# Performance work log

Measured on AMD Instinct MI355X. Metric: run time of the kernel, lower is better.

Reference implementation:

```python
import jax, jax.numpy as jnp
import numpy as np

T = 22        # TypeEncoder.tensor_size() (assumed)
H = 2         # attention heads
C = 64        # hc_graph (per-head out channels)
L = 3         # num_hops
LEAFCAT = 5   # len(LeafType.valid_categories()) (assumed)
NSIZES = 8    # len(LeafType.valid_sizes()) (assumed)
HL = 64       # hc_linear
HT = 64       # hc_task == hc_leafsize
SLOPE = 0.2   # PyG GATConv negative_slope


def _gat(x, src, dst, W, asrc, adst, b):
    # PyG GATConv (concat=True, dropout=0, self-loops already appended to src/dst)
    N = x.shape[0]
    h = (x @ W).reshape(N, H, C)                      # [N,H,C]
    a_s = jnp.einsum('nhc,hc->nh', h, asrc)            # per-node src score
    a_d = jnp.einsum('nhc,hc->nh', h, adst)            # per-node dst score
    e = jax.nn.leaky_relu(a_s[src] + a_d[dst], SLOPE)  # [E+N,H]
    m = jax.ops.segment_max(e, dst, num_segments=N)
    p = jnp.exp(e - m[dst])
    s = jax.ops.segment_sum(p, dst, num_segments=N)
    alpha = p / (s[dst] + 1e-16)                       # scatter-softmax over in-edges
    out = jax.ops.segment_sum(h[src] * alpha[:, :, None], dst, num_segments=N)
    return out.reshape(N, H * C) + b


def _mlp2(z, W1, b1, W2, b2):
    return jax.nn.relu(z @ W1 + b1) @ W2 + b2


def setup_inputs() -> dict:
    key = jax.random.key(0)
    ks = jax.random.split(key, 32)
    N, E, NG, NPG = 102400, 1228800, 256, 400
    D = H * C
    g = lambda k, shp, fan: (jax.random.normal(k, shp, jnp.float32) / np.sqrt(fan)).astype(jnp.float32)
    z = lambda *shp: jnp.zeros(shp, jnp.float32)
    return {
        'x': jax.random.normal(ks[0], (N, D), jnp.float32),
        'edge_index': jax.random.randint(ks[1], (2, E), 0, N),
        'batch': jnp.repeat(jnp.arange(NG, dtype=jnp.int32), NPG),
        'gat_W': g(ks[2], (L, D, D), D),
        'gat_asrc': g(ks[3], (L, H, C), C),
        'gat_adst': g(ks[4], (L, H, C), C),
        'gat_b': z(L, D),
        'shared_W': g(ks[5], (D + T, HL), D + T),
        'shared_b': z(HL),
        'ptr_W1': g(ks[6], (3, HL, HT), HL), 'ptr_b1': z(3, HT),
        'ptr_W2': g(ks[7], (3, HT, 3), HT), 'ptr_b2': z(3, 3),
        'cat_W1': g(ks[8], (HL, HT), HL), 'cat_b1': z(HT),
        'cat_W2': g(ks[9], (HT, LEAFCAT), HT), 'cat_b2': z(LEAFCAT),
        'sf_W1': g(ks[10], (2, HL, HT), HL), 'sf_b1': z(2, HT),
        'sf_W2': g(ks[11], (2, HT, 1), HT), 'sf_b2': z(2, 1),
        'bool_W1': g(ks[12], (HL + T + LEAFCAT + 2, HT), HL + T + LEAFCAT + 2), 'bool_b1': z(HT),
        'bool_W2': g(ks[13], (HT, 1), HT), 'bool_b2': z(1),
        'size_W1': g(ks[14], (HL + T + LEAFCAT + 3, HT), HL + T + LEAFCAT + 3), 'size_b1': z(HT),
        'size_W2': g(ks[15], (HT, NSIZES), HT), 'size_b2': z(NSIZES),
    }


def reference(x, edge_index, batch, gat_W, gat_asrc, gat_adst, gat_b,
              shared_W, shared_b, ptr_W1, ptr_b1, ptr_W2, ptr_b2,
              cat_W1, cat_b1, cat_W2, cat_b2, sf_W1, sf_b1, sf_W2, sf_b2,
              bool_W1, bool_b1, bool_W2, bool_b2, size_W1, size_b1, size_W2, size_b2):
    N = x.shape[0]
    num_graphs = int(batch[-1]) + 1                    # batch is sorted per-graph ids
    node0 = jnp.searchsorted(batch, jnp.arange(num_graphs))  # first node of each graph
    dtype_vec = x[node0, :T]                           # NodeEncoder.split_node_vec dtype slice
    loops = jnp.arange(N)
    src = jnp.concatenate([edge_index[0], loops])      # GATConv add_self_loops=True
    dst = jnp.concatenate([edge_index[1], loops])
    h = x
    for l in range(L):
        h = _gat(h, src, dst, gat_W[l], gat_asrc[l], gat_adst[l], gat_b[l])
        if l < L - 1:
            h = jax.nn.relu(h)
    zf = jax.nn.relu(jnp.concatenate([h[node0], dtype_vec], axis=1) @ shared_W + shared_b)
    # 3 pointer heads, batched
    p = jax.nn.relu(jnp.einsum('gh,khd->kgd', zf, ptr_W1) + ptr_b1[:, None, :])
    ptr = jnp.einsum('kgd,kdo->kgo', p, ptr_W2) + ptr_b2[:, None, :]
    cat_logits = _mlp2(zf, cat_W1, cat_b1, cat_W2, cat_b2)
    q = jax.nn.relu(jnp.einsum('gh,khd->kgd', zf, sf_W1) + sf_b1[:, None, :])
    sf = jnp.einsum('kgd,kdo->kgo', q, sf_W2) + sf_b2[:, None, :]
    signed, floating = sf[0], sf[1]
    bool_in = jnp.concatenate([zf, dtype_vec, cat_logits, signed, floating], axis=1)
    bool_logit = _mlp2(bool_in, bool_W1, bool_b1, bool_W2, bool_b2)
    size_in = jnp.concatenate([bool_in, bool_logit], axis=1)
    size_logits = _mlp2(size_in, size_W1, size_b1, size_W2, size_b2)
    return (ptr[0], ptr[1], ptr[2], cat_logits, signed, floating, bool_logit, size_logits)
```

## Files before the change

kernel.cpp:

```cpp
#include <hip/hip_runtime.h>
#include <hip/hip_bf16.h>

typedef __hip_bfloat16 bf16;
typedef __attribute__((ext_vector_type(8))) short short8;
typedef __attribute__((ext_vector_type(4))) float floatx4;

__device__ __forceinline__ float b2f(bf16 v) { return __bfloat162float(v); }
__device__ __forceinline__ float us2f(unsigned short u) {
    return __uint_as_float(((unsigned)u) << 16);
}
__device__ __forceinline__ unsigned short f2us(float f) {
    bf16 h = __float2bfloat16(f);
    return *(unsigned short*)&h;
}
__device__ __forceinline__ float lo2f(unsigned hv) { return __uint_as_float(hv << 16); }
__device__ __forceinline__ float hi2f(unsigned hv) { return __uint_as_float(hv & 0xffff0000u); }
__device__ __forceinline__ float leaky(float v) { return v > 0.f ? v : 0.2f * v; }

__device__ __forceinline__ float ldw(const void* p, size_t i, int f32) {
    return f32 ? ((const float*)p)[i] : b2f(((const bf16*)p)[i]);
}

template <int F32>
__device__ __forceinline__ float LDWt(const void* p, size_t i) {
    return F32 ? ((const float*)p)[i] : b2f(((const bf16*)p)[i]);
}

__device__ __forceinline__ int or16(const int* f) {
    int r = 0;
#pragma unroll
    for (int j = 0; j < 16; j++) r |= f[j];
    return r;
}

__device__ __forceinline__ float wsum64(float v) {
#pragma unroll
    for (int m = 1; m <= 32; m <<= 1) v += __shfl_xor(v, m);
    return v;
}

__global__ void k_detect_zero(const void* x, int* flagv, char* zbase, size_t zbytes) {
    int b = blockIdx.x;
    int t = threadIdx.x;
    if (b < 16) {
        __shared__ int sbad;
        if (t == 0) sbad = 0;
        __syncthreads();
        float v = b2f(((const bf16*)x)[b * 256 + t]);
        if (!(fabsf(v) < 1e10f)) sbad = 1;
        __syncthreads();
        if (t == 0) flagv[b] = sbad;
    } else {
        size_t off = (size_t)(b - 16) * 4096 + (size_t)t * 16;
        if (off < zbytes) *(uint4*)(zbase + off) = make_uint4(0u, 0u, 0u, 0u);
    }
}

__global__ void k_prep_fused(const void* __restrict__ x, unsigned short* __restrict__ Ab,
                             int nvec,
                             const void* __restrict__ gw, unsigned short* __restrict__ Wt,
                             const void* as_, const void* ad_, const void* b_,
                             float* asF, float* adF, float* bF,
                             const int* __restrict__ batch, int* __restrict__ node0,
                             unsigned char* __restrict__ rootb,
                             unsigned char* __restrict__ flag2, int N,
                             const int* __restrict__ flagv, int nbx8) {
    int b = blockIdx.x;
    int t = threadIdx.x;
    int f32 = or16(flagv);
    if (b < nbx8) {
        int i = b * 256 + t;
        if (i < nvec) {
            if (!f32) {
                ((uint4*)Ab)[i] = ((const uint4*)x)[i];
            } else {
                float4 a = ((const float4*)x)[2 * i];
                float4 c = ((const float4*)x)[2 * i + 1];
                uint4 o;
                o.x = ((unsigned)f2us(a.y) << 16) | f2us(a.x);
                o.y = ((unsigned)f2us(a.w) << 16) | f2us(a.z);
                o.z = ((unsigned)f2us(c.y) << 16) | f2us(c.x);
                o.w = ((unsigned)f2us(c.w) << 16) | f2us(c.z);
                ((uint4*)Ab)[i] = o;
            }
        }
    } else if (b < nbx8 + 192) {
        int i = (b - nbx8) * 256 + t;
        int l = i >> 14, rem = i & 16383, n = rem >> 7, k = rem & 127;
        Wt[i] = f2us(ldw(gw, (size_t)l * 16384 + (size_t)k * 128 + n, f32));
    } else if (b < nbx8 + 194) {
        int i = (b - nbx8 - 192) * 256 + t;
        if (i < 384) {
            asF[i] = ldw(as_, i, f32);
            adF[i] = ldw(ad_, i, f32);
            bF[i] = ldw(b_, i, f32);
        }
    } else {
        int i = (b - nbx8 - 194) * 256 + t;
        if (i < N) {
            int bb = batch[i];
            if (i == 0 || batch[i - 1] != bb) {
                node0[bb] = i;
                rootb[i] = 1;
                flag2[i] = 1;
            }
        }
    }
}

__global__ void k_scan3x(const int* __restrict__ counts,
                         const unsigned char* __restrict__ flag1,
                         const unsigned char* __restrict__ flag2,
                         int* __restrict__ offs, int* __restrict__ wp1, int* __restrict__ wp2,
                         int* __restrict__ bsums, int n) {
    __shared__ int s[256];
    int tid = threadIdx.x;
    int i = blockIdx.x * 256 + tid;
#pragma unroll
    for (int a = 0; a < 3; a++) {
        int v = 0;
        if (i < n) v = (a == 0) ? counts[i] : (a == 1) ? (int)flag1[i] : (int)flag2[i];
        s[tid] = v;
        __syncthreads();
        for (int d = 1; d < 256; d <<= 1) {
            int t2 = (tid >= d) ? s[tid - d] : 0;
            __syncthreads();
            s[tid] += t2;
            __syncthreads();
        }
        int incl = s[tid];
        if (i < n) {
// ... 10 lines not shown
    __shared__ int s[512];
    int tid = threadIdx.x;
#pragma unroll
    for (int a = 0; a < 3; a++) {
        int* arr = bsums + a * 512;
        int v = (tid < nb) ? arr[tid] : 0;
        s[tid] = v;
        __syncthreads();
        for (int d = 1; d < 512; d <<= 1) {
            int t2 = (tid >= d) ? s[tid - d] : 0;
            __syncthreads();
            s[tid] += t2;
            __syncthreads();
        }
        arr[tid] = s[tid] - v;
        if (a >= 1 && tid == 511) nact[a - 1] = s[511];
        __syncthreads();
    }
}

__global__ void k_mark1(const int* __restrict__ ei, const unsigned char* __restrict__ flag2,
                        unsigned char* __restrict__ flag1, int E, int N, int eBlocks) {
    int b = blockIdx.x;
    if (b < eBlocks) {
        int e = b * 256 + threadIdx.x;
        if (e < E && flag2[ei[E + e]]) flag1[ei[e]] = 1;
    } else {
        int i = (b - eBlocks) * 256 + threadIdx.x;
        if (i < N && flag2[i]) flag1[i] = 1;
    }
}

__global__ void k_hist_masked(const int* __restrict__ ei, const unsigned char* __restrict__ flag1,
                              int* __restrict__ counts, int* __restrict__ rank, int E) {
    int e = blockIdx.x * blockDim.x + threadIdx.x;
    if (e < E) {
        int d = ei[E + e];
        if (flag1[d]) rank[e] = atomicAdd(&counts[d], 1);
    }
}

__global__ void k_scatter_wl(const int* __restrict__ ei, const int* __restrict__ offs,
                             const int* __restrict__ bsums, const int* __restrict__ rank,
                             const unsigned char* __restrict__ flag1,
                             const unsigned char* __restrict__ flag2,
                             const int* __restrict__ wp1, const int* __restrict__ wp2,
                             int* __restrict__ adj, int* __restrict__ wl1, int* __restrict__ wl2,
                             int E, int N, int sBlocks) {
    int b = blockIdx.x;
    if (b < sBlocks) {
        int xcd = b & 7;
        int e = (b >> 3) * 256 + threadIdx.x;
        if (e >= E) return;
        int d = ei[E + e];
        if (!flag1[d]) return;
        int lo = (int)(((long long)N * xcd) >> 3);
        int hi = (int)(((long long)N * (xcd + 1)) >> 3);
        if (d >= lo && d < hi) adj[offs[d] + bsums[d >> 8] + rank[e]] = ei[e];
    } else {
        int i = (b - sBlocks) * 256 + threadIdx.x;
        if (i < N) {
            if (flag1[i]) wl1[wp1[i] + bsums[512 + (i >> 8)]] = i;
            if (flag2[i]) wl2[wp2[i] + bsums[1024 + (i >> 8)]] = i;
        }
    }
}

__device__ __forceinline__ void gemm_body(
    const unsigned short* __restrict__ Ab, const unsigned short* __restrict__ Wt,
    unsigned short* __restrict__ Bb, float4* __restrict__ asadv,
    const float* __restrict__ asF, const float* __restrict__ adF, int N,
    const int* __restrict__ wl, const int* __restrict__ nactp, int bb) {
    __shared__ __align__(16) unsigned short Ws[128 * 136];
    __shared__ __align__(16) unsigned short Cs[64 * 136];

    int t = threadIdx.x;
    int r0 = bb * 64;
    int nact = wl ? *nactp : N;
    if (r0 >= nact) return;

    {
        const uint4* src = (const uint4*)Wt;
#pragma unroll
        for (int k = 0; k < 8; k++) {
            int j = t + k * 256;
            int row = j >> 4, c16 = j & 15;
            *(uint4*)&Ws[row * 136 + c16 * 8] = src[j];
        }
    }
    __syncthreads();

    int lane = t & 63;
    int w = t >> 6;
    int ln = lane & 15;
    int quad = lane >> 4;

    int idx = r0 + w * 16 + ln;
    bool valid = idx < nact;
    int arow = idx < N ? idx : N - 1;
    if (wl) arow = valid ? wl[idx] : 0;
    bool wave_active = __any((int)valid);

    if (wave_active) {
        const unsigned short* ap = Ab + (size_t)arow * 128 + quad * 8;

        short8 afrag[4];
        if (valid) {
#pragma unroll
            for (int kt = 0; kt < 4; kt++)
                afrag[kt] = *(const short8*)(ap + kt * 32);
        } else {
#pragma unroll
            for (int kt = 0; kt < 4; kt++)
                afrag[kt] = (short8){0, 0, 0, 0, 0, 0, 0, 0};
        }

        floatx4 acc[8];
#pragma unroll
        for (int nt = 0; nt < 8; nt++) acc[nt] = (floatx4){0.f, 0.f, 0.f, 0.f};

#pragma unroll
        for (int nt = 0; nt < 8; nt++) {
            const unsigned short* wp = Ws + (nt * 16 + ln) * 136 + quad * 8;
#pragma unroll
            for (int kt = 0; kt < 4; kt++) {
                short8 bfrag = *(const short8*)(wp + kt * 32);
                acc[nt] = __builtin_amdgcn_mfma_f32_16x16x32_bf16(afrag[kt], bfrag, acc[nt], 0, 0, 0);
            }
        }

        float as0[4] = {0, 0, 0, 0}, as1[4] = {0, 0, 0, 0};
        float ad0[4] = {0, 0, 0, 0}, ad1[4] = {0, 0, 0, 0};
#pragma unroll
        for (int nt = 0; nt < 8; nt++) {
            float asc = asF[nt * 16 + ln];
            float adc = adF[nt * 16 + ln];
#pragma unroll
            for (int r = 0; r < 4; r++) {
                float v = acc[nt][r];
                Cs[(w * 16 + quad * 4 + r) * 136 + nt * 16 + ln] = f2us(v);
                if (nt < 4) { as0[r] += v * asc; ad0[r] += v * adc; }
                else        { as1[r] += v * asc; ad1[r] += v * adc; }
            }
        }
#pragma unroll
        for (int mask = 1; mask <= 8; mask <<= 1) {
#pragma unroll
            for (int r = 0; r < 4; r++) {
                as0[r] += __shfl_xor(as0[r], mask);
                as1[r] += __shfl_xor(as1[r], mask);
                ad0[r] += __shfl_xor(ad0[r], mask);
                ad1[r] += __shfl_xor(ad1[r], mask);
            }
        }
        if (ln == 0) {
#pragma unroll
            for (int r = 0; r < 4; r++) {
                int idx3 = r0 + w * 16 + quad * 4 + r;
                if (idx3 < nact) {
                    int row = wl ? wl[idx3] : idx3;
// ... 18 lines not shown
}

__global__ __launch_bounds__(256) void k_gemm_mfma(
    const unsigned short* __restrict__ Ab, const unsigned short* __restrict__ Wt,
    unsigned short* __restrict__ Bb, float4* __restrict__ asadv,
    const float* __restrict__ asF, const float* __restrict__ adF, int N,
    const int* __restrict__ wl, const int* __restrict__ nactp) {
    gemm_body(Ab, Wt, Bb, asadv, asF, adF, N, wl, nactp, blockIdx.x);
}

__global__ __launch_bounds__(256) void k_gemm0_mark(
    const unsigned short* __restrict__ Ab, const unsigned short* __restrict__ Wt,
    unsigned short* __restrict__ Bb, float4* __restrict__ asadv,
    const float* __restrict__ asF, const float* __restrict__ adF, int N,
    const int* __restrict__ ei, const unsigned char* __restrict__ rootb,
    unsigned char* __restrict__ flag2, int E, int markBlocks) {
    int b = blockIdx.x;
    if (b < markBlocks) {
        int e = b * 256 + threadIdx.x;
        if (e < E) {
            int d = ei[E + e];
            if (rootb[d]) flag2[ei[e]] = 1;
        }
        return;
    }
    gemm_body(Ab, Wt, Bb, asadv, asF, adF, N, nullptr, nullptr, b - markBlocks);
}

__global__ void k_gat_agg(const uint2* __restrict__ Bu2, const float4* __restrict__ asadv,
                          const int* __restrict__ offs, const int* __restrict__ bsums,
                          const int* __restrict__ counts,
                          const int* __restrict__ adj, const float* __restrict__ biasF,
                          uint2* __restrict__ Au2, float2* __restrict__ pE,
                          const int* __restrict__ nactp, int dorelu,
                          const int* __restrict__ wl) {
    int wave = (blockIdx.x * blockDim.x + threadIdx.x) >> 6;
    int lane = threadIdx.x & 63;
    int hl = lane & 31;
    int hb = lane & 32;
    int idx = wave * 2 + (lane >> 5);
    if (idx >= *nactp) return;
    int node = wl[idx];
    int head = hl >> 4;

    float4 self = asadv[node];
    float ad0 = self.z, ad1 = self.w;
    float es0 = __expf(leaky(self.x + ad0));
    float es1 = __expf(leaky(self.y + ad1));

    int o = offs[node] + bsums[node >> 8];
    int c = counts[node];
    uint2 hvs = Bu2[(size_t)node * 32 + hl];
    float acc0, acc1, acc2, acc3;

    if (c <= 32) {
        int src_r = 0;
        float p0 = 0.f, p1 = 0.f;
        if (hl < c) {
            src_r = adj[o + hl];
            float4 av = asadv[src_r];
            p0 = __expf(leaky(av.x + ad0));
            p1 = __expf(leaky(av.y + ad1));
        }
        float t0 = p0, t1 = p1;
#pragma unroll
        for (int mask = 1; mask <= 16; mask <<= 1) {
            t0 += __shfl_xor(t0, mask);
            t1 += __shfl_xor(t1, mask);
        }
        float inv0 = 1.f / (es0 + t0 + 1e-16f);
        float inv1 = 1.f / (es1 + t1 + 1e-16f);
        p0 *= inv0;
        p1 *= inv1;
        float aself = head ? es1 * inv1 : es0 * inv0;
        acc0 = aself * lo2f(hvs.x);
        acc1 = aself * hi2f(hvs.x);
        acc2 = aself * lo2f(hvs.y);
        acc3 = aself * hi2f(hvs.y);

        uint2 hq[4];
#pragma unroll
        for (int j = 0; j < 4; j++) {
            int s2 = __shfl(src_r, hb + j);
            hq[j] = make_uint2(0u, 0u);
            if (j < c) hq[j] = Bu2[(size_t)s2 * 32 + hl];
        }

        for (int base = 0; base < c; base += 4) {
            uint2 cur[4];
            float av4[4];
#pragma unroll
            for (int j = 0; j < 4; j++) {
                cur[j] = hq[j];
                int idx2 = (base + j) & 31;
                float a0 = __shfl(p0, hb + idx2);
                float a1 = __shfl(p1, hb + idx2);
                float a = head ? a1 : a0;
                av4[j] = (base + j < c) ? a : 0.f;
            }
#pragma unroll
            for (int j = 0; j < 4; j++) {
                int nx = base + 4 + j;
                int s2 = __shfl(src_r, hb + (nx & 31));
                if (nx < c) hq[j] = Bu2[(size_t)s2 * 32 + hl];
            }
#pragma unroll
            for (int j = 0; j < 4; j++) {
                acc0 += av4[j] * lo2f(cur[j].x);
                acc1 += av4[j] * hi2f(cur[j].x);
                acc2 += av4[j] * lo2f(cur[j].y);
                acc3 += av4[j] * hi2f(cur[j].y);
            }
        }
    } else {
        float sum0 = es0, sum1 = es1;
        for (int base = 0; base < c; base += 32) {
            int i = base + hl;
            float p0 = 0.f, p1 = 0.f;
            if (i < c) {
                int s = adj[o + i];
                float4 av = asadv[s];
                p0 = __expf(leaky(av.x + ad0));
                p1 = __expf(leaky(av.y + ad1));
                pE[o + i] = make_float2(p0, p1);
            }
            float t0 = p0, t1 = p1;
#pragma unroll
            for (int mask = 1; mask <= 16; mask <<= 1) {
                t0 += __shfl_xor(t0, mask);
                t1 += __shfl_xor(t1, mask);
            }
            sum0 += t0; sum1 += t1;
        }
        float inv0 = 1.f / (sum0 + 1e-16f);
        float inv1 = 1.f / (sum1 + 1e-16f);
        float aself = head ? es1 * inv1 : es0 * inv0;
        float invh = head ? inv1 : inv0;
        acc0 = aself * lo2f(hvs.x);
        acc1 = aself * hi2f(hvs.x);
        acc2 = aself * lo2f(hvs.y);
        acc3 = aself * hi2f(hvs.y);
        for (int i = 0; i < c; i++) {
            int s = adj[o + i];
            float2 pp = pE[o + i];
            uint2 hv = Bu2[(size_t)s * 32 + hl];
            float a = (head ? pp.y : pp.x) * invh;
            acc0 += a * lo2f(hv.x);
            acc1 += a * hi2f(hv.x);
            acc2 += a * lo2f(hv.y);
            acc3 += a * hi2f(hv.y);
        }
    }

    float4 bb4 = ((const float4*)biasF)[hl];
    float q0 = acc0 + bb4.x;
    float q1 = acc1 + bb4.y;
    float q2 = acc2 + bb4.z;
    float q3 = acc3 + bb4.w;
    if (dorelu) {
        q0 = fmaxf(q0, 0.f); q1 = fmaxf(q1, 0.f);
        q2 = fmaxf(q2, 0.f); q3 = fmaxf(q3, 0.f);
    }
    Au2[(size_t)node * 32 + hl] =
        make_uint2(((unsigned)f2us(q1) << 16) | f2us(q0),
                   ((unsigned)f2us(q3) << 16) | f2us(q2));
}

template <int F32>
__device__ void heads_body(
    const unsigned* __restrict__ Brow, const float4* __restrict__ asadv,
    const int* __restrict__ offs, const int* __restrict__ bsums,
    const int* __restrict__ counts, const int* __restrict__ adj,
    const float* __restrict__ biasF, const int* __restrict__ node0,
    const void* __restrict__ x,
    const void* sW, const void* sb,
    const void* pW1, const void* pb1, const void* pW2, const void* pb2,
    const void* cW1, const void* cb1, const void* cW2, const void* cb2,
    const void* fW1, const void* fb1, const void* fW2, const void* fb2,
    const void* bW1, const void* bb1, const void* bW2, const void* bb2,
    const void* zW1, const void* zb1, const void* zW2, const void* zb2,
    void* __restrict__ outv) {
    int lane = threadIdx.x & 63;
    int g = blockIdx.x * 4 + (threadIdx.x >> 6);
    bf16* outb = (bf16*)outv;
    float* outf = (float*)outv;
#define STORE(idx, val) do { if (F32) outf[idx] = (val); else outb[idx] = __float2bfloat16(val); } while (0)

    int n0 = node0[g];

    float4 self = asadv[n0];
    float es0 = __expf(leaky(self.x + self.z));
    float es1 = __expf(leaky(self.y + self.w));
    int o = offs[n0] + bsums[n0 >> 8];
    int c = counts[n0];

    int srcl = 0;
    float p0 = 0.f, p1 = 0.f;
    if (lane < c) {
        srcl = adj[o + lane];
        float4 av = asadv[srcl];
        p0 = __expf(leaky(av.x + self.z));
        p1 = __expf(leaky(av.y + self.w));
    }
    float sum0 = es0 + wsum64(p0);
    float sum1 = es1 + wsum64(p1);
    for (int base = 64; base < c; base += 64) {
        float q0 = 0.f, q1 = 0.f;
        if (base + lane < c) {
            int s = adj[o + base + lane];
            float4 av = asadv[s];
            q0 = __expf(leaky(av.x + self.z));
            q1 = __expf(leaky(av.y + self.w));
        }
        sum0 += wsum64(q0);
        sum1 += wsum64(q1);
    }
    float inv0 = 1.f / (sum0 + 1e-16f);
    float inv1 = 1.f / (sum1 + 1e-16f);
    float invh = (lane < 32) ? inv0 : inv1;

    unsigned hv0 = Brow[(size_t)n0 * 64 + lane];
    float aself = ((lane < 32) ? es0 : es1) * invh;
    float h0 = aself * lo2f(hv0);
    float h1 = aself * hi2f(hv0);
    int cc = min(c, 64);
    for (int j = 0; j < cc; ++j) {
        int s = __shfl(srcl, j);
        float a0 = __shfl(p0, j);
        float a1 = __shfl(p1, j);
        float aa = ((lane < 32) ? a0 : a1) * invh;
        unsigned hv = Brow[(size_t)s * 64 + lane];
        h0 += aa * lo2f(hv);
        h1 += aa * hi2f(hv);
    }
    for (int j = 64; j < c; ++j) {
        int s = adj[o + j];
        float4 av = asadv[s];
        float aa = (lane < 32) ? __expf(leaky(av.x + self.z)) * inv0
                               : __expf(leaky(av.y + self.w)) * inv1;
        unsigned hv = Brow[(size_t)s * 64 + lane];
        h0 += aa * lo2f(hv);
        h1 += aa * hi2f(hv);
    }
    float2 bias2 = ((const float2*)biasF)[lane];
    h0 += bias2.x;
    h1 += bias2.y;

    float rD = (lane < 22) ? LDWt<F32>(x, (size_t)n0 * 128 + lane) : 0.f;

    float p = 0.f;
    for (int i = 0; i < 64; ++i) {
        p += __shfl(h0, i) * LDWt<F32>(sW, (size_t)(2 * i) * 64 + lane);
        p += __shfl(h1, i) * LDWt<F32>(sW, (size_t)(2 * i + 1) * 64 + lane);
    }
    for (int i = 0; i < 22; ++i)
        p += __shfl(rD, i) * LDWt<F32>(sW, (size_t)(128 + i) * 64 + lane);
    float zf = fmaxf(p + LDWt<F32>(sb, lane), 0.f);

    float bin1 = (lane < 22) ? rD : 0.f;

#pragma unroll
    for (int k = 0; k < 3; ++k) {
        float pp = 0.f;
        for (int i = 0; i < 64; ++i)
            pp += __shfl(zf, i) * LDWt<F32>(pW1, (size_t)k * 4096 + (size_t)i * 64 + lane);
        float tt = fmaxf(pp + LDWt<F32>(pb1, k * 64 + lane), 0.f);
#pragma unroll
        for (int o2 = 0; o2 < 3; ++o2) {
            float v = wsum64(tt * LDWt<F32>(pW2, (size_t)k * 192 + (size_t)lane * 3 + o2));
            if (lane == 0) STORE(k * 768 + g * 3 + o2, v + LDWt<F32>(pb2, k * 3 + o2));
        }
    }

    {
        float pp = 0.f;
        for (int i = 0; i < 64; ++i)
            pp += __shfl(zf, i) * LDWt<F32>(cW1, (size_t)i * 64 + lane);
        float tt = fmaxf(pp + LDWt<F32>(cb1, lane), 0.f);
#pragma unroll
        for (int o2 = 0; o2 < 5; ++o2) {
            float v = wsum64(tt * LDWt<F32>(cW2, (size_t)lane * 5 + o2)) + LDWt<F32>(cb2, o2);
            bin1 = (lane == 22 + o2) ? v : bin1;
            if (lane == 0) STORE(2304 + g * 5 + o2, v);
        }
    }

#pragma unroll
    for (int k = 0; k < 2; ++k) {
        float pp = 0.f;
        for (int i = 0; i < 64; ++i)
            pp += __shfl(zf, i) * LDWt<F32>(fW1, (size_t)k * 4096 + (size_t)i * 64 + lane);
        float tt = fmaxf(pp + LDWt<F32>(fb1, k * 64 + lane), 0.f);
        float v = wsum64(tt * LDWt<F32>(fW2, k * 64 + lane)) + LDWt<F32>(fb2, k);
        bin1 = (lane == 27 + k) ? v : bin1;
        if (lane == 0) STORE(3584 + k * 256 + g, v);
    }

    {
        float pp = 0.f;
        for (int i = 0; i < 64; ++i)
            pp += __shfl(zf, i) * LDWt<F32>(bW1, (size_t)i * 64 + lane);
        for (int i = 0; i < 29; ++i)
            pp += __shfl(bin1, i) * LDWt<F32>(bW1, (size_t)(64 + i) * 64 + lane);
        float tt = fmaxf(pp + LDWt<F32>(bb1, lane), 0.f);
        float v = wsum64(tt * LDWt<F32>(bW2, lane)) + LDWt<F32>(bb2, 0);
        bin1 = (lane == 29) ? v : bin1;
        if (lane == 0) STORE(4096 + g, v);
    }

    {
        float pp = 0.f;
        for (int i = 0; i < 64; ++i)
            pp += __shfl(zf, i) * LDWt<F32>(zW1, (size_t)i * 64 + lane);
        for (int i = 0; i < 30; ++i)
            pp += __shfl(bin1, i) * LDWt<F32>(zW1, (size_t)(64 + i) * 64 + lane);
        float tt = fmaxf(pp + LDWt<F32>(zb1, lane), 0.f);
#pragma unroll
        for (int o2 = 0; o2 < 8; ++o2) {
            float v = wsum64(tt * LDWt<F32>(zW2, (size_t)lane * 8 + o2));
            if (lane == 0) STORE(4352 + g * 8 + o2, v + LDWt<F32>(zb2, o2));
        }
    }
#undef STORE
}

__global__ __launch_bounds__(256) void k_heads2(
    const unsigned* __restrict__ Brow, const float4* __restrict__ asadv,
    const int* __restrict__ offs, const int* __restrict__ bsums,
    const int* __restrict__ counts, const int* __restrict__ adj,
    const float* __restrict__ biasF, const int* __restrict__ node0,
    const void* __restrict__ x,
    const void* sW, const void* sb,
    const void* pW1, const void* pb1, const void* pW2, const void* pb2,
    const void* cW1, const void* cb1, const void* cW2, const void* cb2,
    const void* fW1, const void* fb1, const void* fW2, const void* fb2,
    const void* bW1, const void* bb1, const void* bW2, const void* bb2,
    const void* zW1, const void* zb1, const void* zW2, const void* zb2,
    void* __restrict__ outv, const int* __restrict__ flagv) {
    if (or16(flagv))
        heads_body<1>(Brow, asadv, offs, bsums, counts, adj, biasF, node0, x,
                      sW, sb, pW1, pb1, pW2, pb2, cW1, cb1, cW2, cb2,
                      fW1, fb1, fW2, fb2, bW1, bb1, bW2, bb2,
                      zW1, zb1, zW2, zb2, outv);
    else
        heads_body<0>(Brow, asadv, offs, bsums, counts, adj, biasF, node0, x,
                      sW, sb, pW1, pb1, pW2, pb2, cW1, cb1, cW2, cb2,
                      fW1, fb1, fW2, fb2, bW1, bb1, bW2, bb2,
                      zW1, zb1, zW2, zb2, outv);
}


extern "C" void kernel_launch(void* const* d_in, const int* in_sizes, int n_in,
                              void* d_out, int out_size, void* d_ws, size_t ws_size,
                              hipStream_t stream) {
    const void* x     = d_in[0];
    const int*  ei    = (const int*)d_in[1];
    const int*  batch = (const int*)d_in[2];

    int N = in_sizes[0] / 128;
    int E = in_sizes[1] / 2;

    char* w = (char*)d_ws;
    float4* asad = (float4*)w;              w += (size_t)N * 16;
    unsigned short* A = (unsigned short*)w; w += (size_t)N * 128 * 2;
    unsigned short* B = (unsigned short*)w; w += (size_t)N * 128 * 2;
    float2* pE = (float2*)w;                w += (size_t)E * 8;
    unsigned short* Wt = (unsigned short*)w; w += 3 * 16384 * 2;
    float* asF = (float*)w;                 w += 384 * 4;
    float* adF = (float*)w;                 w += 384 * 4;
    float* bF = (float*)w;                  w += 384 * 4;
    int* offs = (int*)w;                    w += (size_t)N * 4;
    int* wp1 = (int*)w;                     w += (size_t)N * 4;
    int* wp2 = (int*)w;                     w += (size_t)N * 4;
    int* wl1 = (int*)w;                     w += (size_t)N * 4;
    int* wl2 = (int*)w;                     w += (size_t)N * 4;
    int* rank = (int*)w;                    w += (size_t)E * 4;
    int* adj = (int*)w;                     w += (size_t)E * 4;
    int* bsums = (int*)w;                   w += 3 * 512 * 4;
    int* node0 = (int*)w;                   w += 256 * 4;
    int* nact = (int*)w;                    w += 64;
    char* zbase = w;
    int* counts = (int*)w;                  w += (size_t)N * 4;
    unsigned char* flag1 = (unsigned char*)w; w += (size_t)N;
    unsigned char* flag2 = (unsigned char*)w; w += (size_t)N;
    unsigned char* rootb = (unsigned char*)w; w += (size_t)N;
    size_t zbytes = (size_t)N * 7;
    int* flagv = (int*)w;                   w += 64;

    int nb = (N + 255) / 256;
    int nvec = N * 16;
    int nbx8 = (nvec + 255) / 256;
    int nbE = (E + 255) / 256;
    int gemmBlocks = (N + 63) / 64;
    int zBlocks = (int)((zbytes + 4095) / 4096);

    k_detect_zero<<<16 + zBlocks, 256, 0, stream>>>(x, flagv, zbase, zbytes);

    k_prep_fused<<<nbx8 + 194 + nb, 256, 0, stream>>>(
        x, A, nvec, d_in[3], Wt, d_in[4], d_in[5], d_in[6],
        asF, adF, bF, batch, node0, rootb, flag2, N, flagv, nbx8);

    k_gemm0_mark<<<nbE + gemmBlocks, 256, 0, stream>>>(
        A, Wt, B, asad, asF, adF, N, ei, rootb, flag2, E, nbE);

    k_mark1<<<nbE + nb, 256, 0, stream>>>(ei, flag2, flag1, E, N, nbE);

    k_hist_masked<<<nbE, 256, 0, stream>>>(ei, flag1, counts, rank, E);

    k_scan3x<<<nb, 256, 0, stream>>>(counts, flag1, flag2, offs, wp1, wp2, bsums, N);
    k_scan2x<<<1, 512, 0, stream>>>(bsums, nb, nact);

    int sBlocks = 8 * nbE;
    k_scatter_wl<<<sBlocks + nb, 256, 0, stream>>>(
        ei, offs, bsums, rank, flag1, flag2, wp1, wp2, adj, wl1, wl2, E, N, sBlocks);

    int nwaves = (N + 1) / 2;
    int aggblocks = (nwaves + 3) / 4;

    k_gat_agg<<<aggblocks, 256, 0, stream>>>(
        (const uint2*)B, asad, offs, bsums, counts, adj, bF, (uint2*)A, pE,
        nact, 1, wl1);

    k_gemm_mfma<<<gemmBlocks, 256, 0, stream>>>(
        A, Wt + 16384, B, asad, asF + 128, adF + 128, N, wl1, nact);
    k_gat_agg<<<aggblocks, 256, 0, stream>>>(
        (const uint2*)B, asad, offs, bsums, counts, adj, bF + 128, (uint2*)A, pE,
        nact + 1, 1, wl2);

    k_gemm_mfma<<<gemmBlocks, 256, 0, stream>>>(
        A, Wt + 2 * 16384, B, asad, asF + 256, adF + 256, N, wl2, nact + 1);

    k_heads2<<<64, 256, 0, stream>>>(
        (const unsigned*)B, asad, offs, bsums, counts, adj, bF + 256, node0, x,
        d_in[7], d_in[8], d_in[9], d_in[10], d_in[11], d_in[12],
        d_in[13], d_in[14], d_in[15], d_in[16],
        d_in[17], d_in[18], d_in[19], d_in[20],
        d_in[21], d_in[22], d_in[23], d_in[24],
        d_in[25], d_in[26], d_in[27], d_in[28],
        d_out, flagv);
}
```

Baseline: 346.4 us.

## Run output heads as MFMA GEMMs and scatter adjacency with atomic cursors

The per-graph scalar head MLPs become batched bf16 MFMA GEMMs over 64 graphs per block. Head weights are pre-transposed and padded into a bf16 buffer during prep, and the last-layer root aggregation is reused from the generic GAT aggregation kernel writing into a compact buffer. The CSR scatter drops the precomputed rank array and the 8x XCD-partitioned launch in favour of a per-destination atomic cursor. This trades deterministic adjacency order and fp32 head precision for less memory traffic and higher head throughput.

```diff
diff --git a/kernel.cpp b/kernel.cpp
--- a/kernel.cpp
+++ b/kernel.cpp
@@ -5,10 +5,9 @@
 typedef __attribute__((ext_vector_type(8))) short short8;
 typedef __attribute__((ext_vector_type(4))) float floatx4;
 
+#define MF(a, b, c) __builtin_amdgcn_mfma_f32_16x16x32_bf16(a, b, c, 0, 0, 0)
+
 __device__ __forceinline__ float b2f(bf16 v) { return __bfloat162float(v); }
-__device__ __forceinline__ float us2f(unsigned short u) {
-    return __uint_as_float(((unsigned)u) << 16);
-}
 __device__ __forceinline__ unsigned short f2us(float f) {
     bf16 h = __float2bfloat16(f);
     return *(unsigned short*)&h;
@@ -33,10 +32,11 @@
     return r;
 }
 
-__device__ __forceinline__ float wsum64(float v) {
-#pragma unroll
-    for (int m = 1; m <= 32; m <<= 1) v += __shfl_xor(v, m);
-    return v;
+__device__ __forceinline__ void quadred(float part[4]) {
+#pragma unroll
+    for (int m = 1; m <= 8; m <<= 1)
+#pragma unroll
+        for (int r = 0; r < 4; r++) part[r] += __shfl_xor(part[r], m);
 }
 
 __global__ void k_detect_zero(const void* x, int* flagv, char* zbase, size_t zbytes) {
@@ -61,6 +61,9 @@
                              const void* __restrict__ gw, unsigned short* __restrict__ Wt,
                              const void* as_, const void* ad_, const void* b_,
                              float* asF, float* adF, float* bF,
+                             const void* sW_, const void* pW1_, const void* cW1_,
+                             const void* fW1_, const void* bW1_, const void* zW1_,
+                             unsigned short* __restrict__ Whd,
                              const int* __restrict__ batch, int* __restrict__ node0,
                              unsigned char* __restrict__ rootb,
                              unsigned char* __restrict__ flag2, int N,
@@ -95,8 +98,36 @@
             adF[i] = ldw(ad_, i, f32);
             bF[i] = ldw(b_, i, f32);
         }
+    } else if (b < nbx8 + 194 + 184) {
+        int i = (b - nbx8 - 194) * 256 + t;
+        float v;
+        if (i < 10240) {
+            int n = i / 160, k = i - n * 160;
+            v = (k < 150) ? ldw(sW_, (size_t)k * 64 + n, f32) : 0.f;
+        } else if (i < 22528) {
+            int j = i - 10240;
+            int kk = j >> 12, r = j & 4095, n = r >> 6, k = r & 63;
+            v = ldw(pW1_, (size_t)kk * 4096 + (size_t)k * 64 + n, f32);
+        } else if (i < 26624) {
+            int j = i - 22528;
+            int n = j >> 6, k = j & 63;
+            v = ldw(cW1_, (size_t)k * 64 + n, f32);
+        } else if (i < 34816) {
+            int j = i - 26624;
+            int kk = j >> 12, r = j & 4095, n = r >> 6, k = r & 63;
+            v = ldw(fW1_, (size_t)kk * 4096 + (size_t)k * 64 + n, f32);
+        } else if (i < 40960) {
+            int j = i - 34816;
+            int n = j / 96, k = j - n * 96;
+            v = (k < 93) ? ldw(bW1_, (size_t)k * 64 + n, f32) : 0.f;
+        } else {
+            int j = i - 40960;
+            int n = j / 96, k = j - n * 96;
+            v = (k < 94) ? ldw(zW1_, (size_t)k * 64 + n, f32) : 0.f;
+        }
+        Whd[i] = f2us(v);
     } else {
-        int i = (b - nbx8 - 194) * 256 + t;
+        int i = (b - nbx8 - 194 - 184) * 256 + t;
         if (i < N) {
             int bb = batch[i];
             if (i == 0 || batch[i - 1] != bb) {
@@ -173,33 +204,31 @@
 }
 
 __global__ void k_hist_masked(const int* __restrict__ ei, const unsigned char* __restrict__ flag1,
-                              int* __restrict__ counts, int* __restrict__ rank, int E) {
+                              int* __restrict__ counts, int E) {
     int e = blockIdx.x * blockDim.x + threadIdx.x;
     if (e < E) {
         int d = ei[E + e];
-        if (flag1[d]) rank[e] = atomicAdd(&counts[d], 1);
+        if (flag1[d]) atomicAdd(&counts[d], 1);
     }
 }
 
 __global__ void k_scatter_wl(const int* __restrict__ ei, const int* __restrict__ offs,
-                             const int* __restrict__ bsums, const int* __restrict__ rank,
+                             const int* __restrict__ bsums, int* __restrict__ cur,
                              const unsigned char* __restrict__ flag1,
                              const unsigned char* __restrict__ flag2,
                              const int* __restrict__ wp1, const int* __restrict__ wp2,
                              int* __restrict__ adj, int* __restrict__ wl1, int* __restrict__ wl2,
-                             int E, int N, int sBlocks) {
+                             int E, int N, int eBlocks) {
     int b = blockIdx.x;
-    if (b < sBlocks) {
-        int xcd = b & 7;
-        int e = (b >> 3) * 256 + threadIdx.x;
+    if (b < eBlocks) {
+        int e = b * 256 + threadIdx.x;
         if (e >= E) return;
         int d = ei[E + e];
         if (!flag1[d]) return;
-        int lo = (int)(((long long)N * xcd) >> 3);
-        int hi = (int)(((long long)N * (xcd + 1)) >> 3);
-        if (d >= lo && d < hi) adj[offs[d] + bsums[d >> 8] + rank[e]] = ei[e];
+        int r = atomicAdd(&cur[d], 1);
+        adj[offs[d] + bsums[d >> 8] + r] = ei[e];
     } else {
-        int i = (b - sBlocks) * 256 + threadIdx.x;
+        int i = (b - eBlocks) * 256 + threadIdx.x;
         if (i < N) {
             if (flag1[i]) wl1[wp1[i] + bsums[512 + (i >> 8)]] = i;
             if (flag2[i]) wl2[wp2[i] + bsums[1024 + (i >> 8)]] = i;
@@ -266,7 +295,7 @@
 #pragma unroll
             for (int kt = 0; kt < 4; kt++) {
                 short8 bfrag = *(const short8*)(wp + kt * 32);
-                acc[nt] = __builtin_amdgcn_mfma_f32_16x16x32_bf16(afrag[kt], bfrag, acc[nt], 0, 0, 0);
+                acc[nt] = MF(afrag[kt], bfrag, acc[nt]);
             }
         }
 
@@ -351,14 +380,15 @@
                           const int* __restrict__ counts,
                           const int* __restrict__ adj, const float* __restrict__ biasF,
                           uint2* __restrict__ Au2, float2* __restrict__ pE,
-                          const int* __restrict__ nactp, int dorelu,
+                          const int* __restrict__ nactp, int nfix, int dorelu, int byidx,
                           const int* __restrict__ wl) {
     int wave = (blockIdx.x * blockDim.x + threadIdx.x) >> 6;
     int lane = threadIdx.x & 63;
     int hl = lane & 31;
     int hb = lane & 32;
     int idx = wave * 2 + (lane >> 5);
-    if (idx >= *nactp) return;
+    int n = nfix ? nfix : *nactp;
+    if (idx >= n) return;
     int node = wl[idx];
     int head = hl >> 4;
 
@@ -406,11 +436,11 @@
         }
 
         for (int base = 0; base < c; base += 4) {
-            uint2 cur[4];
+            uint2 cu[4];
             float av4[4];
 #pragma unroll
             for (int j = 0; j < 4; j++) {
-                cur[j] = hq[j];
+                cu[j] = hq[j];
                 int idx2 = (base + j) & 31;
                 float a0 = __shfl(p0, hb + idx2);
                 float a1 = __shfl(p1, hb + idx2);
@@ -425,10 +455,10 @@
             }
 #pragma unroll
             for (int j = 0; j < 4; j++) {
-                acc0 += av4[j] * lo2f(cur[j].x);
-                acc1 += av4[j] * hi2f(cur[j].x);
-                acc2 += av4[j] * lo2f(cur[j].y);
-                acc3 += av4[j] * hi2f(cur[j].y);
+                acc0 += av4[j] * lo2f(cu[j].x);
+                acc1 += av4[j] * hi2f(cu[j].x);
+                acc2 += av4[j] * lo2f(cu[j].y);
+                acc3 += av4[j] * hi2f(cu[j].y);
             }
         }
     } else {
@@ -480,192 +510,281 @@
         q0 = fmaxf(q0, 0.f); q1 = fmaxf(q1, 0.f);
         q2 = fmaxf(q2, 0.f); q3 = fmaxf(q3, 0.f);
     }
-    Au2[(size_t)node * 32 + hl] =
+    Au2[(size_t)(byidx ? idx : node) * 32 + hl] =
         make_uint2(((unsigned)f2us(q1) << 16) | f2us(q0),
                    ((unsigned)f2us(q3) << 16) | f2us(q2));
 }
 
 template <int F32>
-__device__ void heads_body(
-    const unsigned* __restrict__ Brow, const float4* __restrict__ asadv,
-    const int* __restrict__ offs, const int* __restrict__ bsums,
-    const int* __restrict__ counts, const int* __restrict__ adj,
-    const float* __restrict__ biasF, const int* __restrict__ node0,
-    const void* __restrict__ x,
-    const void* sW, const void* sb,
-    const void* pW1, const void* pb1, const void* pW2, const void* pb2,
-    const void* cW1, const void* cb1, const void* cW2, const void* cb2,
-    const void* fW1, const void* fb1, const void* fW2, const void* fb2,
-    const void* bW1, const void* bb1, const void* bW2, const void* bb2,
-    const void* zW1, const void* zb1, const void* zW2, const void* zb2,
+__device__ void heads_mfma_body(
+    const unsigned* __restrict__ hroot32, const void* __restrict__ x,
+    const int* __restrict__ node0, const unsigned short* __restrict__ Whd,
+    const void* sb, const void* pb1, const void* pW2, const void* pb2,
+    const void* cb1, const void* cW2, const void* cb2,
+    const void* fb1, const void* fW2, const void* fb2,
+    const void* bb1, const void* bW2, const void* bb2,
+    const void* zb1, const void* zW2, const void* zb2,
     void* __restrict__ outv) {
-    int lane = threadIdx.x & 63;
-    int g = blockIdx.x * 4 + (threadIdx.x >> 6);
+    __shared__ __align__(16) unsigned short hinS[64 * 168];
+    __shared__ __align__(16) unsigned short TwS[4][16 * 168];
+
+    int t = threadIdx.x;
+    int g0b = blockIdx.x * 64;
     bf16* outb = (bf16*)outv;
     float* outf = (float*)outv;
 #define STORE(idx, val) do { if (F32) outf[idx] = (val); else outb[idx] = __float2bfloat16(val); } while (0)
 
-    int n0 = node0[g];
-
-    float4 self = asadv[n0];
-    float es0 = __expf(leaky(self.x + self.z));
-    float es1 = __expf(leaky(self.y + self.w));
-    int o = offs[n0] + bsums[n0 >> 8];
-    int c = counts[n0];
-
-    int srcl = 0;
-    float p0 = 0.f, p1 = 0.f;
-    if (lane < c) {
-        srcl = adj[o + lane];
-        float4 av = asadv[srcl];
-        p0 = __expf(leaky(av.x + self.z));
-        p1 = __expf(leaky(av.y + self.w));
-    }
-    float sum0 = es0 + wsum64(p0);
-    float sum1 = es1 + wsum64(p1);
-    for (int base = 64; base < c; base += 64) {
-        float q0 = 0.f, q1 = 0.f;
-        if (base + lane < c) {
-            int s = adj[o + base + lane];
-            float4 av = asadv[s];
-            q0 = __expf(leaky(av.x + self.z));
-            q1 = __expf(leaky(av.y + self.w));
-        }
-        sum0 += wsum64(q0);
-        sum1 += wsum64(q1);
-    }
-    float inv0 = 1.f / (sum0 + 1e-16f);
-    float inv1 = 1.f / (sum1 + 1e-16f);
-    float invh = (lane < 32) ? inv0 : inv1;
-
-    unsigned hv0 = Brow[(size_t)n0 * 64 + lane];
-    float aself = ((lane < 32) ? es0 : es1) * invh;
-    float h0 = aself * lo2f(hv0);
-    float h1 = aself * hi2f(hv0);
-    int cc = min(c, 64);
-    for (int j = 0; j < cc; ++j) {
-        int s = __shfl(srcl, j);
-        float a0 = __shfl(p0, j);
-        float a1 = __shfl(p1, j);
-        float aa = ((lane < 32) ? a0 : a1) * invh;
-        unsigned hv = Brow[(size_t)s * 64 + lane];
-        h0 += aa * lo2f(hv);
-        h1 += aa * hi2f(hv);
-    }
-    for (int j = 64; j < c; ++j) {
-        int s = adj[o + j];
-        float4 av = asadv[s];
-        float aa = (lane < 32) ? __expf(leaky(av.x + self.z)) * inv0
-                               : __expf(leaky(av.y + self.w)) * inv1;
-        unsigned hv = Brow[(size_t)s * 64 + lane];
-        h0 += aa * lo2f(hv);
-        h1 += aa * hi2f(hv);
-    }
-    float2 bias2 = ((const float2*)biasF)[lane];
-    h0 += bias2.x;
-    h1 += bias2.y;
-
-    float rD = (lane < 22) ? LDWt<F32>(x, (size_t)n0 * 128 + lane) : 0.f;
-
-    float p = 0.f;
-    for (int i = 0; i < 64; ++i) {
-        p += __shfl(h0, i) * LDWt<F32>(sW, (size_t)(2 * i) * 64 + lane);
-        p += __shfl(h1, i) * LDWt<F32>(sW, (size_t)(2 * i + 1) * 64 + lane);
-    }
-    for (int i = 0; i < 22; ++i)
-        p += __shfl(rD, i) * LDWt<F32>(sW, (size_t)(128 + i) * 64 + lane);
-    float zf = fmaxf(p + LDWt<F32>(sb, lane), 0.f);
-
-    float bin1 = (lane < 22) ? rD : 0.f;
-
-#pragma unroll
-    for (int k = 0; k < 3; ++k) {
-        float pp = 0.f;
-        for (int i = 0; i < 64; ++i)
-            pp += __shfl(zf, i) * LDWt<F32>(pW1, (size_t)k * 4096 + (size_t)i * 64 + lane);
-        float tt = fmaxf(pp + LDWt<F32>(pb1, k * 64 + lane), 0.f);
-#pragma unroll
-        for (int o2 = 0; o2 < 3; ++o2) {
-            float v = wsum64(tt * LDWt<F32>(pW2, (size_t)k * 192 + (size_t)lane * 3 + o2));
-            if (lane == 0) STORE(k * 768 + g * 3 + o2, v + LDWt<F32>(pb2, k * 3 + o2));
-        }
-    }
-
     {
-        float pp = 0.f;
-        for (int i = 0; i < 64; ++i)
-            pp += __shfl(zf, i) * LDWt<F32>(cW1, (size_t)i * 64 + lane);
-        float tt = fmaxf(pp + LDWt<F32>(cb1, lane), 0.f);
-#pragma unroll
-        for (int o2 = 0; o2 < 5; ++o2) {
-            float v = wsum64(tt * LDWt<F32>(cW2, (size_t)lane * 5 + o2)) + LDWt<F32>(cb2, o2);
-            bin1 = (lane == 22 + o2) ? v : bin1;
-            if (lane == 0) STORE(2304 + g * 5 + o2, v);
-        }
-    }
-
-#pragma unroll
-    for (int k = 0; k < 2; ++k) {
-        float pp = 0.f;
-        for (int i = 0; i < 64; ++i)
-            pp += __shfl(zf, i) * LDWt<F32>(fW1, (size_t)k * 4096 + (size_t)i * 64 + lane);
-        float tt = fmaxf(pp + LDWt<F32>(fb1, k * 64 + lane), 0.f);
-        float v = wsum64(tt * LDWt<F32>(fW2, k * 64 + lane)) + LDWt<F32>(fb2, k);
-        bin1 = (lane == 27 + k) ? v : bin1;
-        if (lane == 0) STORE(3584 + k * 256 + g, v);
+        unsigned* h32 = (unsigned*)hinS;
+        for (int j = t; j < 64 * 64; j += 256) {
+            int gl = j >> 6, c = j & 63;
+            h32[gl * 84 + c] = hroot32[(size_t)(g0b + gl) * 64 + c];
+        }
+        for (int j = t; j < 64 * 20; j += 256) {
+            int gl = j / 20, c = j - gl * 20;
+            int n0 = node0[g0b + gl];
+            int k0 = 2 * c;
+            float d0 = (k0 < 22) ? LDWt<F32>(x, (size_t)n0 * 128 + k0) : 0.f;
+            float d1 = (k0 + 1 < 22) ? LDWt<F32>(x, (size_t)n0 * 128 + k0 + 1) : 0.f;
+            h32[gl * 84 + 64 + c] = ((unsigned)f2us(d1) << 16) | f2us(d0);
+        }
+    }
+    __syncthreads();
+
+    int w = t >> 6;
+    int lane = t & 63;
+    int ln = lane & 15, quad = lane >> 4;
+    unsigned short* T = TwS[w];
+    int gq = quad * 4;
+    int gw0 = g0b + w * 16;
+
+    for (int j = lane; j < 16 * 32; j += 64) {
+        int gl = j >> 5, c = j & 31;
+        T[gl * 168 + 64 + c] =
+            (c < 22) ? hinS[(w * 16 + gl) * 168 + 128 + c] : (unsigned short)0;
+    }
+
+    short8 afA[5];
+#pragma unroll
+    for (int kt = 0; kt < 5; kt++)
+        afA[kt] = *(const short8*)&hinS[(w * 16 + ln) * 168 + quad * 8 + kt * 32];
+#pragma unroll
+    for (int nt = 0; nt < 4; nt++) {
+        floatx4 acc = (floatx4){0.f, 0.f, 0.f, 0.f};
+        const unsigned short* bp = Whd + (nt * 16 + ln) * 160 + quad * 8;
+#pragma unroll
+        for (int kt = 0; kt < 5; kt++)
+            acc = MF(afA[kt], *(const short8*)(bp + kt * 32), acc);
+        float bias = LDWt<F32>(sb, nt * 16 + ln);
+#pragma unroll
+        for (int r = 0; r < 4; r++)
+            T[(gq + r) * 168 + nt * 16 + ln] = f2us(fmaxf(acc[r] + bias, 0.f));
+    }
+    __syncthreads();
+
+    short8 af20 = *(const short8*)&T[ln * 168 + quad * 8];
+    short8 af21 = *(const short8*)&T[ln * 168 + quad * 8 + 32];
+
+#pragma unroll
+    for (int k = 0; k < 3; k++) {
+        const unsigned short* Bw = Whd + 10240 + k * 4096;
+        floatx4 acc[4];
+#pragma unroll
+        for (int nt = 0; nt < 4; nt++) {
+            floatx4 a = (floatx4){0.f, 0.f, 0.f, 0.f};
+            const unsigned short* bp = Bw + (nt * 16 + ln) * 64 + quad * 8;
+            a = MF(af20, *(const short8*)bp, a);
+            a = MF(af21, *(const short8*)(bp + 32), a);
+            float b1 = LDWt<F32>(pb1, k * 64 + nt * 16 + ln);
+#pragma unroll
+            for (int r = 0; r < 4; r++) a[r] = fmaxf(a[r] + b1, 0.f);
+            acc[nt] = a;
+        }
+#pragma unroll
+        for (int o = 0; o < 3; o++) {
+            float w2[4], part[4];
+#pragma unroll
+            for (int nt = 0; nt < 4; nt++)
+                w2[nt] = LDWt<F32>(pW2, (size_t)k * 192 + (size_t)(nt * 16 + ln) * 3 + o);
+#pragma unroll
+            for (int r = 0; r < 4; r++)
+                part[r] = acc[0][r] * w2[0] + acc[1][r] * w2[1] +
+                          acc[2][r] * w2[2] + acc[3][r] * w2[3];
+            quadred(part);
+            if (ln == 0) {
+                float b2 = LDWt<F32>(pb2, k * 3 + o);
+#pragma unroll
+                for (int r = 0; r < 4; r++)
+                    STORE(k * 768 + (gw0 + gq + r) * 3 + o, part[r] + b2);
+            }
+        }
     }
 
     {
-        float pp = 0.f;
-        for (int i = 0; i < 64; ++i)
-            pp += __shfl(zf, i) * LDWt<F32>(bW1, (size_t)i * 64 + lane);
-        for (int i = 0; i < 29; ++i)
-            pp += __shfl(bin1, i) * LDWt<F32>(bW1, (size_t)(64 + i) * 64 + lane);
-        float tt = fmaxf(pp + LDWt<F32>(bb1, lane), 0.f);
-        float v = wsum64(tt * LDWt<F32>(bW2, lane)) + LDWt<F32>(bb2, 0);
-        bin1 = (lane == 29) ? v : bin1;
-        if (lane == 0) STORE(4096 + g, v);
-    }
+        const unsigned short* Bw = Whd + 22528;
+        floatx4 acc[4];
+#pragma unroll
+        for (int nt = 0; nt < 4; nt++) {
+            floatx4 a = (floatx4){0.f, 0.f, 0.f, 0.f};
+            const unsigned short* bp = Bw + (nt * 16 + ln) * 64 + quad * 8;
+            a = MF(af20, *(const short8*)bp, a);
+            a = MF(af21, *(const short8*)(bp + 32), a);
+            float b1 = LDWt<F32>(cb1, nt * 16 + ln);
+#pragma unroll
+            for (int r = 0; r < 4; r++) a[r] = fmaxf(a[r] + b1, 0.f);
+            acc[nt] = a;
+        }
+#pragma unroll
+        for (int o = 0; o < 5; o++) {
+            float w2[4], part[4];
+#pragma unroll
+            for (int nt = 0; nt < 4; nt++)
+                w2[nt] = LDWt<F32>(cW2, (size_t)(nt * 16 + ln) * 5 + o);
+#pragma unroll
+            for (int r = 0; r < 4; r++)
+                part[r] = acc[0][r] * w2[0] + acc[1][r] * w2[1] +
+                          acc[2][r] * w2[2] + acc[3][r] * w2[3];
+            quadred(part);
+            if (ln == 0) {
+                float b2 = LDWt<F32>(cb2, o);
+#pragma unroll
+                for (int r = 0; r < 4; r++) {
+                    float v = part[r] + b2;
+                    T[(gq + r) * 168 + 86 + o] = f2us(v);
+                    STORE(2304 + (gw0 + gq + r) * 5 + o, v);
+                }
+            }
+        }
+    }
+
+#pragma unroll
+    for (int k = 0; k < 2; k++) {
+        const unsigned short* Bw = Whd + 26624 + k * 4096;
+        floatx4 acc[4];
+#pragma unroll
+        for (int nt = 0; nt < 4; nt++) {
+            floatx4 a = (floatx4){0.f, 0.f, 0.f, 0.f};
+            const unsigned short* bp = Bw + (nt * 16 + ln) * 64 + quad * 8;
+            a = MF(af20, *(const short8*)bp, a);
+            a = MF(af21, *(const short8*)(bp + 32), a);
+            float b1 = LDWt<F32>(fb1, k * 64 + nt * 16 + ln);
+#pragma unroll
+            for (int r = 0; r < 4; r++) a[r] = fmaxf(a[r] + b1, 0.f);
+            acc[nt] = a;
+        }
+        float w2[4], part[4];
+#pragma unroll
+        for (int nt = 0; nt < 4; nt++)
+            w2[nt] = LDWt<F32>(fW2, (size_t)k * 64 + nt * 16 + ln);
+#pragma unroll
+        for (int r = 0; r < 4; r++)
+            part[r] = acc[0][r] * w2[0] + acc[1][r] * w2[1] +
+                      acc[2][r] * w2[2] + acc[3][r] * w2[3];
+        quadred(part);
+        if (ln == 0) {
+            float b2 = LDWt<F32>(fb2, k);
+#pragma unroll
+            for (int r = 0; r < 4; r++) {
+                float v = part[r] + b2;
+                T[(gq + r) * 168 + 91 + k] = f2us(v);
+                STORE(3584 + k * 256 + (gw0 + gq + r), v);
+            }
+        }
+    }
+    __syncthreads();
+
+    short8 af3 = *(const short8*)&T[ln * 168 + 64 + quad * 8];
 
     {
-        float pp = 0.f;
-        for (int i = 0; i < 64; ++i)
-            pp += __shfl(zf, i) * LDWt<F32>(zW1, (size_t)i * 64 + lane);
-        for (int i = 0; i < 30; ++i)
-            pp += __shfl(bin1, i) * LDWt<F32>(zW1, (size_t)(64 + i) * 64 + lane);
-        float tt = fmaxf(pp + LDWt<F32>(zb1, lane), 0.f);
-#pragma unroll
-        for (int o2 = 0; o2 < 8; ++o2) {
-            float v = wsum64(tt * LDWt<F32>(zW2, (size_t)lane * 8 + o2));
-            if (lane == 0) STORE(4352 + g * 8 + o2, v + LDWt<F32>(zb2, o2));
+        const unsigned short* Bw = Whd + 34816;
+        floatx4 acc[4];
+#pragma unroll
+        for (int nt = 0; nt < 4; nt++) {
+            floatx4 a = (floatx4){0.f, 0.f, 0.f, 0.f};
+            const unsigned short* bp = Bw + (nt * 16 + ln) * 96 + quad * 8;
+            a = MF(af20, *(const short8*)bp, a);
+            a = MF(af21, *(const short8*)(bp + 32), a);
+            a = MF(af3, *(const short8*)(bp + 64), a);
+            float b1 = LDWt<F32>(bb1, nt * 16 + ln);
+#pragma unroll
+            for (int r = 0; r < 4; r++) a[r] = fmaxf(a[r] + b1, 0.f);
+            acc[nt] = a;
+        }
+        float w2[4], part[4];
+#pragma unroll
+        for (int nt = 0; nt < 4; nt++)
+            w2[nt] = LDWt<F32>(bW2, nt * 16 + ln);
+#pragma unroll
+        for (int r = 0; r < 4; r++)
+            part[r] = acc[0][r] * w2[0] + acc[1][r] * w2[1] +
+                      acc[2][r] * w2[2] + acc[3][r] * w2[3];
+        quadred(part);
+        if (ln == 0) {
+            float b2 = LDWt<F32>(bb2, 0);
+#pragma unroll
+            for (int r = 0; r < 4; r++) {
+                float v = part[r] + b2;
+                T[(gq + r) * 168 + 93] = f2us(v);
+                STORE(4096 + (gw0 + gq + r), v);
+            }
+        }
+    }
+    __syncthreads();
+
+    af3 = *(const short8*)&T[ln * 168 + 64 + quad * 8];
+
+    {
+        const unsigned short* Bw = Whd + 40960;
+        floatx4 acc[4];
+#pragma unroll
+        for (int nt = 0; nt < 4; nt++) {
+            floatx4 a = (floatx4){0.f, 0.f, 0.f, 0.f};
+            const unsigned short* bp = Bw + (nt * 16 + ln) * 96 + quad * 8;
+            a = MF(af20, *(const short8*)bp, a);
+            a = MF(af21, *(const short8*)(bp + 32), a);
+            a = MF(af3, *(const short8*)(bp + 64), a);
+            float b1 = LDWt<F32>(zb1, nt * 16 + ln);
+#pragma unroll
+            for (int r = 0; r < 4; r++) a[r] = fmaxf(a[r] + b1, 0.f);
+            acc[nt] = a;
+        }
+#pragma unroll
+        for (int o = 0; o < 8; o++) {
+            float w2[4], part[4];
+#pragma unroll
+            for (int nt = 0; nt < 4; nt++)
+                w2[nt] = LDWt<F32>(zW2, (size_t)(nt * 16 + ln) * 8 + o);
+#pragma unroll
+            for (int r = 0; r < 4; r++)
+                part[r] = acc[0][r] * w2[0] + acc[1][r] * w2[1] +
+                          acc[2][r] * w2[2] + acc[3][r] * w2[3];
+            quadred(part);
+            if (ln == 0) {
+                float b2 = LDWt<F32>(zb2, o);
+#pragma unroll
+                for (int r = 0; r < 4; r++)
+                    STORE(4352 + (gw0 + gq + r) * 8 + o, part[r] + b2);
+            }
         }
     }
 #undef STORE
 }
 
-__global__ __launch_bounds__(256) void k_heads2(
-    const unsigned* __restrict__ Brow, const float4* __restrict__ asadv,
-    const int* __restrict__ offs, const int* __restrict__ bsums,
-    const int* __restrict__ counts, const int* __restrict__ adj,
-    const float* __restrict__ biasF, const int* __restrict__ node0,
-    const void* __restrict__ x,
-    const void* sW, const void* sb,
-    const void* pW1, const void* pb1, const void* pW2, const void* pb2,
-    const void* cW1, const void* cb1, const void* cW2, const void* cb2,
-    const void* fW1, const void* fb1, const void* fW2, const void* fb2,
-    const void* bW1, const void* bb1, const void* bW2, const void* bb2,
-    const void* zW1, const void* zb1, const void* zW2, const void* zb2,
+__global__ __launch_bounds__(256) void k_heads_mfma(
+    const unsigned* __restrict__ hroot32, const void* __restrict__ x,
+    const int* __restrict__ node0, const unsigned short* __restrict__ Whd,
+    const void* sb, const void* pb1, const void* pW2, const void* pb2,
+    const void* cb1, const void* cW2, const void* cb2,
+    const void* fb1, const void* fW2, const void* fb2,
+    const void* bb1, const void* bW2, const void* bb2,
+    const void* zb1, const void* zW2, const void* zb2,
     void* __restrict__ outv, const int* __restrict__ flagv) {
     if (or16(flagv))
-        heads_body<1>(Brow, asadv, offs, bsums, counts, adj, biasF, node0, x,
-                      sW, sb, pW1, pb1, pW2, pb2, cW1, cb1, cW2, cb2,
-                      fW1, fb1, fW2, fb2, bW1, bb1, bW2, bb2,
-                      zW1, zb1, zW2, zb2, outv);
+        heads_mfma_body<1>(hroot32, x, node0, Whd, sb, pb1, pW2, pb2, cb1, cW2, cb2,
+                           fb1, fW2, fb2, bb1, bW2, bb2, zb1, zW2, zb2, outv);
     else
-        heads_body<0>(Brow, asadv, offs, bsums, counts, adj, biasF, node0, x,
-                      sW, sb, pW1, pb1, pW2, pb2, cW1, cb1, cW2, cb2,
-                      fW1, fb1, fW2, fb2, bW1, bb1, bW2, bb2,
-                      zW1, zb1, zW2, zb2, outv);
+        heads_mfma_body<0>(hroot32, x, node0, Whd, sb, pb1, pW2, pb2, cb1, cW2, cb2,
+                           fb1, fW2, fb2, bb1, bW2, bb2, zb1, zW2, zb2, outv);
 }
 
 
@@ -685,6 +804,7 @@
     unsigned short* B = (unsigned short*)w; w += (size_t)N * 128 * 2;
     float2* pE = (float2*)w;                w += (size_t)E * 8;
     unsigned short* Wt = (unsigned short*)w; w += 3 * 16384 * 2;
+    unsigned short* Whd = (unsigned short*)w; w += 47104 * 2;
     float* asF = (float*)w;                 w += 384 * 4;
     float* adF = (float*)w;                 w += 384 * 4;
     float* bF = (float*)w;                  w += 384 * 4;
@@ -693,17 +813,18 @@
     int* wp2 = (int*)w;                     w += (size_t)N * 4;
     int* wl1 = (int*)w;                     w += (size_t)N * 4;
     int* wl2 = (int*)w;                     w += (size_t)N * 4;
-    int* rank = (int*)w;                    w += (size_t)E * 4;
     int* adj = (int*)w;                     w += (size_t)E * 4;
     int* bsums = (int*)w;                   w += 3 * 512 * 4;
     int* node0 = (int*)w;                   w += 256 * 4;
     int* nact = (int*)w;                    w += 64;
+    unsigned* hroot = (unsigned*)w;         w += 256 * 128 * 2;
     char* zbase = w;
     int* counts = (int*)w;                  w += (size_t)N * 4;
+    int* cur = (int*)w;                     w += (size_t)N * 4;
     unsigned char* flag1 = (unsigned char*)w; w += (size_t)N;
     unsigned char* flag2 = (unsigned char*)w; w += (size_t)N;
     unsigned char* rootb = (unsigned char*)w; w += (size_t)N;
-    size_t zbytes = (size_t)N * 7;
+    size_t zbytes = (size_t)N * 11;
     int* flagv = (int*)w;                   w += 64;
 
     int nb = (N + 255) / 256;
@@ -715,46 +836,51 @@
 
     k_detect_zero<<<16 + zBlocks, 256, 0, stream>>>(x, flagv, zbase, zbytes);
 
-    k_prep_fused<<<nbx8 + 194 + nb, 256, 0, stream>>>(
+    k_prep_fused<<<nbx8 + 194 + 184 + nb, 256, 0, stream>>>(
         x, A, nvec, d_in[3], Wt, d_in[4], d_in[5], d_in[6],
-        asF, adF, bF, batch, node0, rootb, flag2, N, flagv, nbx8);
+        asF, adF, bF,
+        d_in[7], d_in[9], d_in[13], d_in[17], d_in[21], d_in[25], Whd,
+        batch, node0, rootb, flag2, N, flagv, nbx8);
 
     k_gemm0_mark<<<nbE + gemmBlocks, 256, 0, stream>>>(
         A, Wt, B, asad, asF, adF, N, ei, rootb, flag2, E, nbE);
 
     k_mark1<<<nbE + nb, 256, 0, stream>>>(ei, flag2, flag1, E, N, nbE);
 
-    k_hist_masked<<<nbE, 256, 0, stream>>>(ei, flag1, counts, rank, E);
+    k_hist_masked<<<nbE, 256, 0, stream>>>(ei, flag1, counts, E);
 
     k_scan3x<<<nb, 256, 0, stream>>>(counts, flag1, flag2, offs, wp1, wp2, bsums, N);
     k_scan2x<<<1, 512, 0, stream>>>(bsums, nb, nact);
 
-    int sBlocks = 8 * nbE;
-    k_scatter_wl<<<sBlocks + nb, 256, 0, stream>>>(
-        ei, offs, bsums, rank, flag1, flag2, wp1, wp2, adj, wl1, wl2, E, N, sBlocks);
+    k_scatter_wl<<<nbE + nb, 256, 0, stream>>>(
+        ei, offs, bsums, cur, flag1, flag2, wp1, wp2, adj, wl1, wl2, E, N, nbE);
 
     int nwaves = (N + 1) / 2;
     int aggblocks = (nwaves + 3) / 4;
 
     k_gat_agg<<<aggblocks, 256, 0, stream>>>(
         (const uint2*)B, asad, offs, bsums, counts, adj, bF, (uint2*)A, pE,
-        nact, 1, wl1);
+        nact, 0, 1, 0, wl1);
 
     k_gemm_mfma<<<gemmBlocks, 256, 0, stream>>>(
         A, Wt + 16384, B, asad, asF + 128, adF + 128, N, wl1, nact);
     k_gat_agg<<<aggblocks, 256, 0, stream>>>(
         (const uint2*)B, asad, offs, bsums, counts, adj, bF + 128, (uint2*)A, pE,
-        nact + 1, 1, wl2);
+        nact + 1, 0, 1, 0, wl2);
 
     k_gemm_mfma<<<gemmBlocks, 256, 0, stream>>>(
         A, Wt + 2 * 16384, B, asad, asF + 256, adF + 256, N, wl2, nact + 1);
 
-    k_heads2<<<64, 256, 0, stream>>>(
-        (const unsigned*)B, asad, offs, bsums, counts, adj, bF + 256, node0, x,
-        d_in[7], d_in[8], d_in[9], d_in[10], d_in[11], d_in[12],
-        d_in[13], d_in[14], d_in[15], d_in[16],
-        d_in[17], d_in[18], d_in[19], d_in[20],
-        d_in[21], d_in[22], d_in[23], d_in[24],
-        d_in[25], d_in[26], d_in[27], d_in[28],
+    k_gat_agg<<<32, 256, 0, stream>>>(
+        (const uint2*)B, asad, offs, bsums, counts, adj, bF + 256, (uint2*)hroot, pE,
+        nact, 256, 0, 1, node0);
+
+    k_heads_mfma<<<4, 256, 0, stream>>>(
+        hroot, x, node0, Whd,
+        d_in[8], d_in[10], d_in[11], d_in[12],
+        d_in[14], d_in[15], d_in[16],
+        d_in[18], d_in[19], d_in[20],
+        d_in[22], d_in[23], d_in[24],
+        d_in[26], d_in[27], d_in[28],
         d_out, flagv);
 }
```

After: 316.4 us. -8.7%, faster.
